# Kernel tuning notes

Measured on AMD Instinct MI355X. Metric: run time of the kernel, lower is better.

The kernel has to match this reference:

```python
import jax, jax.numpy as jnp
import numpy as np

N = 131072
F = 128
T = 256          # number of distinct transformer ids (all present w.h.p.)
K = 5            # max_clusters_per_transformer
TC = T * K       # total_clusters


def setup_inputs() -> dict:
    key = jax.random.key(0)
    k1, k2, k3, k4, k5, k6 = jax.random.split(key, 6)
    x = jax.random.normal(k1, (N, F), dtype=jnp.float32)
    transformer_ids = jax.random.randint(k2, (N,), 0, T, dtype=jnp.int64)
    # MLP params: Linear(F, F//2) -> ReLU -> Linear(F//2, K)
    H = F // 2
    lim1 = 1.0 / np.sqrt(F)
    lim2 = 1.0 / np.sqrt(H)
    W1 = jax.random.uniform(k3, (F, H), minval=-lim1, maxval=lim1, dtype=jnp.float32)
    b1 = jax.random.uniform(k4, (H,), minval=-lim1, maxval=lim1, dtype=jnp.float32)
    W2 = jax.random.uniform(k5, (H, K), minval=-lim2, maxval=lim2, dtype=jnp.float32)
    b2 = jax.random.uniform(k6, (K,), minval=-lim2, maxval=lim2, dtype=jnp.float32)
    return {"x": x, "transformer_ids": transformer_ids,
            "W1": W1, "b1": b1, "W2": W2, "b2": b2}


def reference(x, transformer_ids, W1, b1, W2, b2):
    # Shared MLP + softmax over all nodes (equivalent to the per-group loop,
    # since local_assign weights are shared across groups).
    h = jax.nn.relu(x @ W1 + b1)               # [N, F//2]
    P = jax.nn.softmax(h @ W2 + b2, axis=1)    # [N, K]
    # Scatter each node's K probabilities into its group's column block.
    # With ids uniform over [0, T), unique(ids) == arange(T), so the block
    # offset for node n is transformer_ids[n] * K.
    cols = transformer_ids[:, None] * K + jnp.arange(K)[None, :]   # [N, K]
    rows = jnp.arange(N)[:, None]                                   # [N, 1]
    S = jnp.zeros((N, TC), dtype=P.dtype).at[rows, cols].set(P)     # [N, TC]
    cluster_ids = jnp.argmax(S, axis=1)                             # [N]
    return S, cluster_ids
```

## Files before the change

kernel.cpp:

```cpp
#include <hip/hip_runtime.h>


constexpr int kN   = 131072;
constexpr int kF   = 128;
constexpr int kH   = 64;
constexpr int kK   = 5;
constexpr int kTC  = 1280;
constexpr int ROWS = 256;
constexpr int BLK  = 256;

typedef float f32x4 __attribute__((ext_vector_type(4)));

__global__ __launch_bounds__(BLK, 2)
void tcp_compute(const float* __restrict__ x,
                 const int*   __restrict__ tids,
                 const float* __restrict__ W1,
                 const float* __restrict__ b1,
                 const float* __restrict__ W2,
                 const float* __restrict__ b2,
                 float* __restrict__ out)
{
    const int tid = threadIdx.x;
    const long long row = (long long)blockIdx.x * ROWS + tid;

    float h[kH];
#pragma unroll
    for (int j = 0; j < kH; ++j) h[j] = b1[j];

    const f32x4* x4 = reinterpret_cast<const f32x4*>(x + row * kF);
#pragma unroll 2
    for (int f4 = 0; f4 < kF / 4; ++f4) {
        const f32x4 xv = x4[f4];
#pragma unroll
        for (int e = 0; e < 4; ++e) {
            const float xs = xv[e];
            const float* w = W1 + (f4 * 4 + e) * kH;
#pragma unroll
            for (int j = 0; j < kH; ++j)
                h[j] = fmaf(xs, w[j], h[j]);
        }
    }
#pragma unroll
    for (int j = 0; j < kH; ++j) h[j] = fmaxf(h[j], 0.0f);

    float lg[kK];
#pragma unroll
    for (int k = 0; k < kK; ++k) lg[k] = b2[k];
#pragma unroll 8
    for (int j = 0; j < kH; ++j) {
        const float* w = W2 + j * kK;
#pragma unroll
        for (int k = 0; k < kK; ++k)
            lg[k] = fmaf(h[j], w[k], lg[k]);
    }

    float m = lg[0];
#pragma unroll
    for (int k = 1; k < kK; ++k) m = fmaxf(m, lg[k]);
    float p[kK];
    float ssum = 0.0f;
#pragma unroll
    for (int k = 0; k < kK; ++k) { p[k] = expf(lg[k] - m); ssum += p[k]; }
#pragma unroll
    for (int k = 0; k < kK; ++k) p[k] = p[k] / ssum;

    int am = 0; float best = p[0];
#pragma unroll
    for (int k = 1; k < kK; ++k) if (p[k] > best) { best = p[k]; am = k; }

    const int c0 = tids[row] * kK;

    float* srow = out + row * (long long)kTC + c0;
#pragma unroll
    for (int k = 0; k < kK; ++k) srow[k] = p[k];

    out[(long long)kN * kTC + row] = (float)(c0 + am);
}

extern "C" void kernel_launch(void* const* d_in, const int* in_sizes, int n_in,
                              void* d_out, int out_size, void* d_ws, size_t ws_size,
                              hipStream_t stream) {
    const float* x  = (const float*)d_in[0];
    const int* tids = (const int*)d_in[1];
    const float* W1 = (const float*)d_in[2];
    const float* b1 = (const float*)d_in[3];
    const float* W2 = (const float*)d_in[4];
    const float* b2 = (const float*)d_in[5];
    float* out = (float*)d_out;

    hipMemsetAsync(d_out, 0, (size_t)kN * kTC * sizeof(float), stream);

    dim3 grid(kN / ROWS);
    dim3 block(BLK);
    hipLaunchKernelGGL(tcp_compute, grid, block, 0, stream,
                       x, tids, W1, b1, W2, b2, out);
}
```

Before: 913.2 us.

## Tile first MLP layer through shared memory with register-blocked outer products

Stage W1, W2 and transposed x tiles in LDS. Each of 512 threads computes an 8-row by 4-column block of the hidden layer, then 256 threads finish the second layer, softmax and scatter. This replaces per-thread 64-wide accumulation from global memory with register-blocked reuse. The large LDS footprint limits residency to about one block per CU.

```diff
diff --git a/kernel.cpp b/kernel.cpp
--- a/kernel.cpp
+++ b/kernel.cpp
@@ -7,74 +7,125 @@
 constexpr int kK   = 5;
 constexpr int kTC  = 1280;
 constexpr int ROWS = 256;
-constexpr int BLK  = 256;
+constexpr int BLK  = 512;
 
 typedef float f32x4 __attribute__((ext_vector_type(4)));
 
-__global__ __launch_bounds__(BLK, 2)
-void tcp_compute(const float* __restrict__ x,
-                 const int*   __restrict__ tids,
-                 const float* __restrict__ W1,
-                 const float* __restrict__ b1,
-                 const float* __restrict__ W2,
-                 const float* __restrict__ b2,
-                 float* __restrict__ out)
+__global__ __launch_bounds__(BLK)
+void tcp_fused(const float* __restrict__ x,
+               const int*   __restrict__ tids,
+               const float* __restrict__ W1,
+               const float* __restrict__ b1,
+               const float* __restrict__ W2,
+               const float* __restrict__ b2,
+               float* __restrict__ out)
 {
+    __shared__ float buf[17408];
+    __shared__ float W1s[128 * 64];
+    __shared__ float W2s[64 * 8];
+    __shared__ float b2s[8];
+
     const int tid = threadIdx.x;
-    const long long row = (long long)blockIdx.x * ROWS + tid;
+    const int i   = tid & 31;
+    const int jj  = tid >> 5;
+    const long long brow = (long long)blockIdx.x * ROWS;
 
-    float h[kH];
+    {
+        const f32x4* g = reinterpret_cast<const f32x4*>(W1);
+        f32x4* s = reinterpret_cast<f32x4*>(W1s);
 #pragma unroll
-    for (int j = 0; j < kH; ++j) h[j] = b1[j];
+        for (int q = 0; q < 4; ++q) s[tid + q * BLK] = g[tid + q * BLK];
+    }
+    if (tid < 320) W2s[(tid / 5) * 8 + (tid % 5)] = W2[tid];
+    if (tid < 5)   b2s[tid] = b2[tid];
 
-    const f32x4* x4 = reinterpret_cast<const f32x4*>(x + row * kF);
-#pragma unroll 2
-    for (int f4 = 0; f4 < kF / 4; ++f4) {
-        const f32x4 xv = x4[f4];
+    float bv[4];
 #pragma unroll
-        for (int e = 0; e < 4; ++e) {
-            const float xs = xv[e];
-            const float* w = W1 + (f4 * 4 + e) * kH;
+    for (int c = 0; c < 4; ++c) bv[c] = b1[jj * 4 + c];
+    float acc[8][4];
 #pragma unroll
-            for (int j = 0; j < kH; ++j)
-                h[j] = fmaf(xs, w[j], h[j]);
+    for (int k = 0; k < 8; ++k)
+#pragma unroll
+        for (int c = 0; c < 4; ++c) acc[k][c] = bv[c];
+
+    const f32x4* x4g = reinterpret_cast<const f32x4*>(x);
+
+    for (int half = 0; half < 2; ++half) {
+        __syncthreads();
+#pragma unroll
+        for (int q = 0; q < 8; ++q) {
+            const int idx = q * BLK + tid;
+            const int row = idx >> 4;
+            const int f4  = idx & 15;
+            const f32x4 v = x4g[(brow + row) * 32 + half * 16 + f4];
+#pragma unroll
+            for (int e = 0; e < 4; ++e)
+                buf[(f4 * 4 + e) * 257 + row] = v[e];
+        }
+        __syncthreads();
+        for (int fh = 0; fh < 64; ++fh) {
+            const f32x4 wv =
+                *reinterpret_cast<const f32x4*>(&W1s[(half * 64 + fh) * 64 + jj * 4]);
+            float xv[8];
+#pragma unroll
+            for (int k = 0; k < 8; ++k) xv[k] = buf[fh * 257 + i + 32 * k];
+#pragma unroll
+            for (int k = 0; k < 8; ++k)
+#pragma unroll
+                for (int c = 0; c < 4; ++c)
+                    acc[k][c] = fmaf(xv[k], wv[c], acc[k][c]);
         }
     }
+
+    __syncthreads();
 #pragma unroll
-    for (int j = 0; j < kH; ++j) h[j] = fmaxf(h[j], 0.0f);
+    for (int k = 0; k < 8; ++k) {
+        f32x4 hv;
+#pragma unroll
+        for (int c = 0; c < 4; ++c) hv[c] = fmaxf(acc[k][c], 0.0f);
+        *reinterpret_cast<f32x4*>(&buf[(i + 32 * k) * 68 + jj * 4]) = hv;
+    }
+    __syncthreads();
 
-    float lg[kK];
+    if (tid < ROWS) {
+        const int row = tid;
+        const long long grow = brow + row;
+        float hr[64];
 #pragma unroll
-    for (int k = 0; k < kK; ++k) lg[k] = b2[k];
+        for (int c4 = 0; c4 < 16; ++c4) {
+            const f32x4 v = *reinterpret_cast<const f32x4*>(&buf[row * 68 + c4 * 4]);
+#pragma unroll
+            for (int e = 0; e < 4; ++e) hr[c4 * 4 + e] = v[e];
+        }
+        f32x4 lgv = {b2s[0], b2s[1], b2s[2], b2s[3]};
+        float lg4 = b2s[4];
 #pragma unroll 8
-    for (int j = 0; j < kH; ++j) {
-        const float* w = W2 + j * kK;
+        for (int j = 0; j < 64; ++j) {
+            const float hj = hr[j];
+            const f32x4 wv = *reinterpret_cast<const f32x4*>(&W2s[j * 8]);
 #pragma unroll
-        for (int k = 0; k < kK; ++k)
-            lg[k] = fmaf(h[j], w[k], lg[k]);
+            for (int c = 0; c < 4; ++c) lgv[c] = fmaf(hj, wv[c], lgv[c]);
+            lg4 = fmaf(hj, W2s[j * 8 + 4], lg4);
+        }
+        float lg[kK] = {lgv[0], lgv[1], lgv[2], lgv[3], lg4};
+        float m = lg[0];
+#pragma unroll
+        for (int k = 1; k < kK; ++k) m = fmaxf(m, lg[k]);
+        float p[kK]; float ssum = 0.0f;
+#pragma unroll
+        for (int k = 0; k < kK; ++k) { p[k] = expf(lg[k] - m); ssum += p[k]; }
+#pragma unroll
+        for (int k = 0; k < kK; ++k) p[k] = p[k] / ssum;
+        int am = 0; float best = p[0];
+#pragma unroll
+        for (int k = 1; k < kK; ++k) if (p[k] > best) { best = p[k]; am = k; }
+
+        const int c0 = tids[grow] * kK;
+        float* srow = out + grow * (long long)kTC + c0;
+#pragma unroll
+        for (int k = 0; k < kK; ++k) srow[k] = p[k];
+        out[(long long)kN * kTC + grow] = (float)(c0 + am);
     }
-
-    float m = lg[0];
-#pragma unroll
-    for (int k = 1; k < kK; ++k) m = fmaxf(m, lg[k]);
-    float p[kK];
-    float ssum = 0.0f;
-#pragma unroll
-    for (int k = 0; k < kK; ++k) { p[k] = expf(lg[k] - m); ssum += p[k]; }
-#pragma unroll
-    for (int k = 0; k < kK; ++k) p[k] = p[k] / ssum;
-
-    int am = 0; float best = p[0];
-#pragma unroll
-    for (int k = 1; k < kK; ++k) if (p[k] > best) { best = p[k]; am = k; }
-
-    const int c0 = tids[row] * kK;
-
-    float* srow = out + row * (long long)kTC + c0;
-#pragma unroll
-    for (int k = 0; k < kK; ++k) srow[k] = p[k];
-
-    out[(long long)kN * kTC + row] = (float)(c0 + am);
 }
 
 extern "C" void kernel_launch(void* const* d_in, const int* in_sizes, int n_in,
@@ -92,6 +143,6 @@
 
     dim3 grid(kN / ROWS);
     dim3 block(BLK);
-    hipLaunchKernelGGL(tcp_compute, grid, block, 0, stream,
+    hipLaunchKernelGGL(tcp_fused, grid, block, 0, stream,
                        x, tids, W1, b1, W2, b2, out);
 }
```

Measured after the change: 750.9 us. 1.22x faster.
